# Performance work log

Hardware: AMD Instinct MI355X
Metric: run time of the kernel (lower is better)

The kernel has to match this reference:

```python
import jax, jax.numpy as jnp
import numpy as np

B, C, H, W_ = 64, 3, 224, 224
S = 196            # max_segments
MP = 400           # max_pixels_per_segment
D = 768            # embed_dim (vit_base)


def setup_inputs() -> dict:
    key = jax.random.key(0)
    k1, k2, k3 = jax.random.split(key, 3)
    img = jax.random.normal(k1, (B, C, H, W_), jnp.float32)
    segments = jax.random.randint(k2, (B, H, W_), 0, S, jnp.int32)
    W = jax.random.normal(k3, (C * MP, D), jnp.float32) * 0.02
    b = jnp.zeros((D,), jnp.float32)
    return {"img": img, "segments": segments, "W": W, "b": b}


def _embed_one(img_chw, seg_hw):
    """Gather up to MP pixels per segment (row-major order, like torch bool-mask
    indexing), zero-pad, and flatten in (C, MP) order. Returns [S, C*MP]."""
    c = img_chw.shape[0]
    P = H * W_
    seg = seg_hw.reshape(-1)                                   # [P]
    order = jnp.argsort(seg, stable=True)                      # pixels sorted by segment, row-major within segment
    sorted_seg = seg[order]
    counts = jax.ops.segment_sum(jnp.ones((P,), jnp.int32), seg, num_segments=S)
    starts = jnp.concatenate([jnp.zeros((1,), jnp.int32),
                              jnp.cumsum(counts)[:-1].astype(jnp.int32)])
    rank = jnp.arange(P, dtype=jnp.int32) - starts[sorted_seg]  # index within segment
    valid = rank < MP                                           # truncate overflow pixels
    safe_rank = jnp.minimum(rank, MP - 1)
    pix = img_chw.reshape(c, P).T[order]                        # [P, C]
    buf = jnp.zeros((S, MP, c), img_chw.dtype)
    # (segment, rank) pairs are unique for valid pixels; overflow adds zeros
    buf = buf.at[sorted_seg, safe_rank].add(pix * valid[:, None].astype(img_chw.dtype))
    # torch flattens (C, MP) row-major -> channel-major feature layout
    return buf.transpose(0, 2, 1).reshape(S, c * MP)


def reference(img, segments, W, b):
    feats = jax.vmap(_embed_one)(img, segments)  # [B, S, C*MP]
    return feats @ W + b                          # [B, S, D]
```

## Files before the change

kernel.cpp:

```cpp
#include <hip/hip_runtime.h>
#include <hip/hip_bf16.h>
#include <stdint.h>

#define BATCH 64
#define CHN 3
#define HH 224
#define WW 224
#define PIX (HH * WW)
#define NSEG 196
#define MAXP 400
#define KDIM (CHN * MAXP)
#define DN 768

#define KP4 1216
#define NTK 38
#define MROWS (BATCH * NSEG)

#define CHSZ 512
#define NCH (PIX / CHSZ)

typedef short short8 __attribute__((ext_vector_type(8)));
typedef float f32x4 __attribute__((ext_vector_type(4)));
typedef unsigned int uint4v __attribute__((ext_vector_type(4)));


__device__ __forceinline__ uint32_t packhl(float v) {
    uint32_t x = __float_as_uint(v);
    uint32_t hi = (x + 0x7FFFu + ((x >> 16) & 1u)) >> 16;
    float r = v - __uint_as_float(hi << 16);
    uint32_t y = __float_as_uint(r);
    uint32_t lo = (y + 0x7FFFu + ((y >> 16) & 1u)) >> 16;
    return (hi << 16) | lo;
}

__global__ void k_hist(const int* __restrict__ seg, int* __restrict__ hist) {
    __shared__ int cnt[NSEG];
    int blk = blockIdx.x;
    int b = blk / NCH, ch = blk % NCH;
    int tid = threadIdx.x;
    if (tid < NSEG) cnt[tid] = 0;
    __syncthreads();
    int s = seg[(size_t)b * PIX + ch * CHSZ + tid];
    atomicAdd(&cnt[s], 1);
    __syncthreads();
    if (tid < NSEG) hist[(size_t)blk * NSEG + tid] = cnt[tid];
}

__global__ void k_scan(int* __restrict__ hist, int* __restrict__ counts) {
    int i = blockIdx.x * blockDim.x + threadIdx.x;
    if (i >= BATCH * NSEG) return;
    int b = i / NSEG, s = i % NSEG;
    int run = 0;
    for (int c = 0; c < NCH; ++c) {
        size_t idx = ((size_t)b * NCH + c) * NSEG + s;
        int t = hist[idx];
        hist[idx] = run;
        run += t;
    }
    counts[i] = run;
}

__global__ void k_ztail(const int* __restrict__ counts, uint32_t* __restrict__ Apair) {
    int row = blockIdx.x * 4 + (threadIdx.x >> 6);
    int lane = threadIdx.x & 63;
    int cnt = counts[row];
    int start = 3 * min(cnt, MAXP);
    uint32_t* p = Apair + (size_t)row * KP4;
    for (int i = start + lane; i < KP4; i += 64) p[i] = 0u;
}

__global__ void k_scatter(const float* __restrict__ img,
                          const int* __restrict__ seg,
                          const int* __restrict__ offs,
                          uint32_t* __restrict__ Apair) {
    __shared__ int soff[NSEG];
    __shared__ int wcnt[8][NSEG];
    int blk = blockIdx.x;
    int b = blk / NCH, ch = blk % NCH;
    int tid = threadIdx.x;
    int lane = tid & 63, wid = tid >> 6;

    for (int i = tid; i < 8 * NSEG; i += CHSZ) ((int*)wcnt)[i] = 0;
    if (tid < NSEG) soff[tid] = offs[(size_t)blk * NSEG + tid];
    __syncthreads();

    int p = ch * CHSZ + tid;
    int sv = seg[(size_t)b * PIX + p];

    uint64_t m = ~0ull;
    #pragma unroll
    for (int bit = 0; bit < 8; ++bit) {
        uint64_t bal = __ballot((sv >> bit) & 1);
        m &= ((sv >> bit) & 1) ? bal : ~bal;
    }
    int before = __popcll(m & ((1ull << lane) - 1ull));
    int first  = __builtin_ctzll(m);
    if (lane == first) wcnt[wid][sv] = __popcll(m);
    __syncthreads();

    int base = soff[sv];
    for (int w2 = 0; w2 < wid; ++w2) base += wcnt[w2][sv];
    int r = base + before;

    if (r < MAXP) {
        const float* ib = img + (size_t)b * CHN * PIX + p;
        uint32_t* dst = Apair + (size_t)(b * NSEG + sv) * KP4 + 3 * r;
        uint32_t v0 = packhl(ib[0]);
        uint32_t v1 = packhl(ib[PIX]);
        uint32_t v2 = packhl(ib[2 * PIX]);
        dst[0] = v0; dst[1] = v1; dst[2] = v2;
    }
}

__global__ void k_wprep(const float* __restrict__ W, uint32_t* __restrict__ Wt) {
    __shared__ float t[32][33];
    int kt = blockIdx.x, nt = blockIdx.y;
    int tid = threadIdx.x;
    int tx = tid & 31, ty = tid >> 5;
    #pragma unroll
    for (int i = 0; i < 4; ++i) {
        int k = kt * 32 + i * 8 + ty;
        int n = nt * 32 + tx;
        t[i * 8 + ty][tx] = (k < KDIM) ? W[(size_t)k * DN + n] : 0.0f;
    }
    __syncthreads();
    #pragma unroll
    for (int i = 0; i < 4; ++i) {
        int n = nt * 32 + i * 8 + ty;
        int k = kt * 32 + tx;
        int kap = (k < KDIM) ? 3 * (k % MAXP) + (k / MAXP) : k;
        Wt[(size_t)n * KP4 + kap] = packhl(t[tx][i * 8 + ty]);
    }
}

__device__ __forceinline__ void gld16(const void* g, void* l) {
    __builtin_amdgcn_global_load_lds(
        (const __attribute__((address_space(1))) unsigned int*)g,
        (__attribute__((address_space(3))) unsigned int*)l, 16, 0, 0);
}

#define NWG 588
__global__ __launch_bounds__(256) void k_gemm(const uint32_t* __restrict__ A,
                                              const uint32_t* __restrict__ Bw,
                                              const float* __restrict__ bias,
                                              float* __restrict__ Co) {
    __shared__ uint32_t lds[2][2][128 * 32];
    int j = blockIdx.x;
    int xcd = j & 7, sl = j >> 3;
    const int q = NWG / 8, rm = NWG % 8;
    int wgid = (xcd < rm ? xcd * (q + 1) : rm * (q + 1) + (xcd - rm) * q) + sl;
    int bm = wgid / 6, bn = wgid % 6;

    int tid = threadIdx.x;
    int lane = tid & 63, w = tid >> 6;
    int wm = w >> 1, wn = w & 1;
    int srow = lane >> 3, sslot = lane & 7;
    int kb = lane >> 4, r15 = lane & 15;

    const uint32_t* Abase = A + (size_t)(bm * 128) * KP4;
    const uint32_t* Bbase = Bw + (size_t)(bn * 128) * KP4;

    f32x4 acc[4][4] = {};

#define STAGE(buf, kt) do {                                                   \
    _Pragma("unroll")                                                         \
    for (int qq = 0; qq < 4; ++qq) {                                          \
        int rb = (qq * 4 + w) * 8;                                            \
        int row = rb + srow;                                                  \
        int sp = sslot ^ (row & 7);                                           \
        gld16(Abase + (size_t)row * KP4 + (kt) * 32 + sp * 4,                 \
              &lds[buf][0][rb * 32]);                                         \
        gld16(Bbase + (size_t)row * KP4 + (kt) * 32 + sp * 4,                 \
              &lds[buf][1][rb * 32]);                                         \
    }                                                                         \
} while (0)

    STAGE(0, 0);
    __syncthreads();

    int cur = 0;
    for (int kt = 0; kt < NTK; ++kt) {
        if (kt + 1 < NTK) STAGE(cur ^ 1, kt + 1);

        short8 ah[4], al[4], bh[4], bl[4];
        #pragma unroll
        for (int mi = 0; mi < 4; ++mi) {
            int row = wm * 64 + mi * 16 + r15;
            int s0 = (2 * kb) ^ (row & 7), s1 = (2 * kb + 1) ^ (row & 7);
            uint4v w0 = *(const uint4v*)&lds[cur][0][row * 32 + s0 * 4];
            uint4v w1 = *(const uint4v*)&lds[cur][0][row * 32 + s1 * 4];
            union { uint32_t u[4]; short8 s; } H, L;
            H.u[0] = __builtin_amdgcn_perm(w0.y, w0.x, 0x07060302u);
            H.u[1] = __builtin_amdgcn_perm(w0.w, w0.z, 0x07060302u);
            H.u[2] = __builtin_amdgcn_perm(w1.y, w1.x, 0x07060302u);
            H.u[3] = __builtin_amdgcn_perm(w1.w, w1.z, 0x07060302u);
            L.u[0] = __builtin_amdgcn_perm(w0.y, w0.x, 0x05040100u);
            L.u[1] = __builtin_amdgcn_perm(w0.w, w0.z, 0x05040100u);
            L.u[2] = __builtin_amdgcn_perm(w1.y, w1.x, 0x05040100u);
            L.u[3] = __builtin_amdgcn_perm(w1.w, w1.z, 0x05040100u);
            ah[mi] = H.s; al[mi] = L.s;
        }
        #pragma unroll
        for (int ni = 0; ni < 4; ++ni) {
            int row = wn * 64 + ni * 16 + r15;
            int s0 = (2 * kb) ^ (row & 7), s1 = (2 * kb + 1) ^ (row & 7);
            uint4v w0 = *(const uint4v*)&lds[cur][1][row * 32 + s0 * 4];
            uint4v w1 = *(const uint4v*)&lds[cur][1][row * 32 + s1 * 4];
            union { uint32_t u[4]; short8 s; } H, L;
            H.u[0] = __builtin_amdgcn_perm(w0.y, w0.x, 0x07060302u);
            H.u[1] = __builtin_amdgcn_perm(w0.w, w0.z, 0x07060302u);
            H.u[2] = __builtin_amdgcn_perm(w1.y, w1.x, 0x07060302u);
            H.u[3] = __builtin_amdgcn_perm(w1.w, w1.z, 0x07060302u);
            L.u[0] = __builtin_amdgcn_perm(w0.y, w0.x, 0x05040100u);
            L.u[1] = __builtin_amdgcn_perm(w0.w, w0.z, 0x05040100u);
            L.u[2] = __builtin_amdgcn_perm(w1.y, w1.x, 0x05040100u);
            L.u[3] = __builtin_amdgcn_perm(w1.w, w1.z, 0x05040100u);
            bh[ni] = H.s; bl[ni] = L.s;
        }

        #pragma unroll
        for (int mi = 0; mi < 4; ++mi)
            #pragma unroll
            for (int ni = 0; ni < 4; ++ni) {
                acc[mi][ni] = __builtin_amdgcn_mfma_f32_16x16x32_bf16(
                    ah[mi], bh[ni], acc[mi][ni], 0, 0, 0);
                acc[mi][ni] = __builtin_amdgcn_mfma_f32_16x16x32_bf16(
                    al[mi], bh[ni], acc[mi][ni], 0, 0, 0);
                acc[mi][ni] = __builtin_amdgcn_mfma_f32_16x16x32_bf16(
                    ah[mi], bl[ni], acc[mi][ni], 0, 0, 0);
            }

        __syncthreads();
        cur ^= 1;
    }
#undef STAGE

    #pragma unroll
    for (int ni = 0; ni < 4; ++ni) {
        int col = bn * 128 + wn * 64 + ni * 16 + r15;
        float bv = bias[col];
        #pragma unroll
        for (int mi = 0; mi < 4; ++mi) {
            int rbase = bm * 128 + wm * 64 + mi * 16 + kb * 4;
            #pragma unroll
            for (int e = 0; e < 4; ++e)
                Co[(size_t)(rbase + e) * DN + col] = acc[mi][ni][e] + bv;
        }
    }
}

extern "C" void kernel_launch(void* const* d_in, const int* in_sizes, int n_in,
                              void* d_out, int out_size, void* d_ws, size_t ws_size,
                              hipStream_t stream) {
    const float* img = (const float*)d_in[0];
    const int*   seg = (const int*)d_in[1];
    const float* W   = (const float*)d_in[2];
    const float* bia = (const float*)d_in[3];
    float* out = (float*)d_out;

    const size_t APAIR_BYTES = (size_t)MROWS * KP4 * 4;
    const size_t HIST_BYTES  = (size_t)BATCH * NCH * NSEG * 4;
    uint32_t* Apair  = (uint32_t*)d_ws;
    int*      hist   = (int*)((char*)d_ws + APAIR_BYTES);
    int*      counts = (int*)((char*)d_ws + APAIR_BYTES + HIST_BYTES);
    uint32_t* Wt     = (uint32_t*)hist;

    k_hist<<<BATCH * NCH, CHSZ, 0, stream>>>(seg, hist);
    k_scan<<<(BATCH * NSEG + 255) / 256, 256, 0, stream>>>(hist, counts);
    k_ztail<<<MROWS / 4, 256, 0, stream>>>(counts, Apair);
    k_scatter<<<BATCH * NCH, CHSZ, 0, stream>>>(img, seg, hist, Apair);
    k_wprep<<<dim3(NTK, DN / 32), 256, 0, stream>>>(W, Wt);

    k_gemm<<<NWG, 256, 0, stream>>>(Apair, Wt, bia, out);
}
```

Before: 236.7 us.

## Restructure split-bf16 GEMM with half-swap MFMA pairing, parallel scan, XCD-remapped scatter

The GEMM now uses 512 threads (8 waves, 4x2 tiles each). It feeds the packed hi/lo bf16 words straight to MFMA, paired with a half-swapped B operand, so two MFMAs per tile give the full (ah+al)(bh+bl) product. This removes all the perm unpacking instructions but adds the al*bl term and changes the MFMA count and register pressure. The prefix scan changes from one thread per segment walking the chunks serially to one wavefront per segment using shuffle-based scans. The scatter kernel remaps block indices so neighbouring chunks land on the same XCD.

```diff
diff --git a/kernel.cpp b/kernel.cpp
--- a/kernel.cpp
+++ b/kernel.cpp
@@ -47,17 +47,23 @@
 }
 
 __global__ void k_scan(int* __restrict__ hist, int* __restrict__ counts) {
-    int i = blockIdx.x * blockDim.x + threadIdx.x;
-    if (i >= BATCH * NSEG) return;
-    int b = i / NSEG, s = i % NSEG;
-    int run = 0;
-    for (int c = 0; c < NCH; ++c) {
-        size_t idx = ((size_t)b * NCH + c) * NSEG + s;
-        int t = hist[idx];
-        hist[idx] = run;
-        run += t;
-    }
-    counts[i] = run;
+    int gw = blockIdx.x * 4 + (threadIdx.x >> 6);
+    int lane = threadIdx.x & 63;
+    int b = gw / NSEG, s = gw - b * NSEG;
+    size_t base = (size_t)b * NCH * NSEG + s;
+    int v0 = hist[base + (size_t)lane * NSEG];
+    int v1 = (lane < NCH - 64) ? hist[base + (size_t)(lane + 64) * NSEG] : 0;
+    int p0 = v0, p1 = v1;
+    #pragma unroll
+    for (int d = 1; d < 64; d <<= 1) {
+        int t0 = __shfl_up(p0, d);
+        int t1 = __shfl_up(p1, d);
+        if (lane >= d) { p0 += t0; p1 += t1; }
+    }
+    int tot0 = __shfl(p0, 63);
+    hist[base + (size_t)lane * NSEG] = p0 - v0;
+    if (lane < NCH - 64) hist[base + (size_t)(lane + 64) * NSEG] = tot0 + p1 - v1;
+    if (lane == NCH - 64 - 1) counts[gw] = tot0 + p1;
 }
 
 __global__ void k_ztail(const int* __restrict__ counts, uint32_t* __restrict__ Apair) {
@@ -75,13 +81,14 @@
                           uint32_t* __restrict__ Apair) {
     __shared__ int soff[NSEG];
     __shared__ int wcnt[8][NSEG];
-    int blk = blockIdx.x;
-    int b = blk / NCH, ch = blk % NCH;
+    int blk0 = blockIdx.x;
+    int wg = (blk0 & 7) * (BATCH * NCH / 8) + (blk0 >> 3);
+    int b = wg / NCH, ch = wg % NCH;
     int tid = threadIdx.x;
     int lane = tid & 63, wid = tid >> 6;
 
     for (int i = tid; i < 8 * NSEG; i += CHSZ) ((int*)wcnt)[i] = 0;
-    if (tid < NSEG) soff[tid] = offs[(size_t)blk * NSEG + tid];
+    if (tid < NSEG) soff[tid] = offs[(size_t)wg * NSEG + tid];
     __syncthreads();
 
     int p = ch * CHSZ + tid;
@@ -140,10 +147,10 @@
 }
 
 #define NWG 588
-__global__ __launch_bounds__(256) void k_gemm(const uint32_t* __restrict__ A,
-                                              const uint32_t* __restrict__ Bw,
-                                              const float* __restrict__ bias,
-                                              float* __restrict__ Co) {
+__global__ __launch_bounds__(512, 4) void k_gemm(const uint32_t* __restrict__ A,
+                                                 const uint32_t* __restrict__ Bw,
+                                                 const float* __restrict__ bias,
+                                                 float* __restrict__ Co) {
     __shared__ uint32_t lds[2][2][128 * 32];
     int j = blockIdx.x;
     int xcd = j & 7, sl = j >> 3;
@@ -153,26 +160,25 @@
 
     int tid = threadIdx.x;
     int lane = tid & 63, w = tid >> 6;
-    int wm = w >> 1, wn = w & 1;
-    int srow = lane >> 3, sslot = lane & 7;
-    int kb = lane >> 4, r15 = lane & 15;
-
-    const uint32_t* Abase = A + (size_t)(bm * 128) * KP4;
-    const uint32_t* Bbase = Bw + (size_t)(bn * 128) * KP4;
-
-    f32x4 acc[4][4] = {};
-
-#define STAGE(buf, kt) do {                                                   \
-    _Pragma("unroll")                                                         \
-    for (int qq = 0; qq < 4; ++qq) {                                          \
-        int rb = (qq * 4 + w) * 8;                                            \
-        int row = rb + srow;                                                  \
-        int sp = sslot ^ (row & 7);                                           \
-        gld16(Abase + (size_t)row * KP4 + (kt) * 32 + sp * 4,                 \
-              &lds[buf][0][rb * 32]);                                         \
-        gld16(Bbase + (size_t)row * KP4 + (kt) * 32 + sp * 4,                 \
-              &lds[buf][1][rb * 32]);                                         \
-    }                                                                         \
+    int wm = w >> 2, wn = w & 3;
+    int r15 = lane & 15, kb = lane >> 4;
+
+    int srow = w * 8 + (lane >> 3);
+    int sslot = lane & 7;
+    int ssw = sslot ^ (srow & 7);
+    size_t aoff0 = (size_t)srow * KP4 + ssw * 4;
+    size_t aoff1 = (size_t)(srow + 64) * KP4 + ssw * 4;
+
+    const uint32_t* Ab = A + (size_t)(bm * 128) * KP4;
+    const uint32_t* Bb = Bw + (size_t)(bn * 128) * KP4;
+
+    f32x4 acc[4][2] = {};
+
+#define STAGE(buf, kt) do {                                        \
+    gld16(Ab + aoff0 + (size_t)(kt) * 32, &lds[buf][0][w * 256]);  \
+    gld16(Ab + aoff1 + (size_t)(kt) * 32, &lds[buf][0][2048 + w * 256]); \
+    gld16(Bb + aoff0 + (size_t)(kt) * 32, &lds[buf][1][w * 256]);  \
+    gld16(Bb + aoff1 + (size_t)(kt) * 32, &lds[buf][1][2048 + w * 256]); \
 } while (0)
 
     STAGE(0, 0);
@@ -182,53 +188,34 @@
     for (int kt = 0; kt < NTK; ++kt) {
         if (kt + 1 < NTK) STAGE(cur ^ 1, kt + 1);
 
-        short8 ah[4], al[4], bh[4], bl[4];
         #pragma unroll
-        for (int mi = 0; mi < 4; ++mi) {
-            int row = wm * 64 + mi * 16 + r15;
-            int s0 = (2 * kb) ^ (row & 7), s1 = (2 * kb + 1) ^ (row & 7);
-            uint4v w0 = *(const uint4v*)&lds[cur][0][row * 32 + s0 * 4];
-            uint4v w1 = *(const uint4v*)&lds[cur][0][row * 32 + s1 * 4];
-            union { uint32_t u[4]; short8 s; } H, L;
-            H.u[0] = __builtin_amdgcn_perm(w0.y, w0.x, 0x07060302u);
-            H.u[1] = __builtin_amdgcn_perm(w0.w, w0.z, 0x07060302u);
-            H.u[2] = __builtin_amdgcn_perm(w1.y, w1.x, 0x07060302u);
-            H.u[3] = __builtin_amdgcn_perm(w1.w, w1.z, 0x07060302u);
-            L.u[0] = __builtin_amdgcn_perm(w0.y, w0.x, 0x05040100u);
-            L.u[1] = __builtin_amdgcn_perm(w0.w, w0.z, 0x05040100u);
-            L.u[2] = __builtin_amdgcn_perm(w1.y, w1.x, 0x05040100u);
-            L.u[3] = __builtin_amdgcn_perm(w1.w, w1.z, 0x05040100u);
-            ah[mi] = H.s; al[mi] = L.s;
+        for (int sg = 0; sg < 2; ++sg) {
+            union { uint4v u; short8 s; } af[4];
+            #pragma unroll
+            for (int mi = 0; mi < 4; ++mi) {
+                int row = wm * 64 + mi * 16 + r15;
+                int slot = (sg * 4 + kb) ^ (row & 7);
+                af[mi].u = *(const uint4v*)&lds[cur][0][row * 32 + slot * 4];
+            }
+            #pragma unroll
+            for (int ni = 0; ni < 2; ++ni) {
+                int row = wn * 32 + ni * 16 + r15;
+                int slot = (sg * 4 + kb) ^ (row & 7);
+                union { uint4v u; short8 s; } bf, bs;
+                bf.u = *(const uint4v*)&lds[cur][1][row * 32 + slot * 4];
+                bs.u.x = (bf.u.x >> 16) | (bf.u.x << 16);
+                bs.u.y = (bf.u.y >> 16) | (bf.u.y << 16);
+                bs.u.z = (bf.u.z >> 16) | (bf.u.z << 16);
+                bs.u.w = (bf.u.w >> 16) | (bf.u.w << 16);
+                #pragma unroll
+                for (int mi = 0; mi < 4; ++mi) {
+                    acc[mi][ni] = __builtin_amdgcn_mfma_f32_16x16x32_bf16(
+                        af[mi].s, bf.s, acc[mi][ni], 0, 0, 0);
+                    acc[mi][ni] = __builtin_amdgcn_mfma_f32_16x16x32_bf16(
+                        af[mi].s, bs.s, acc[mi][ni], 0, 0, 0);
+                }
+            }
         }
-        #pragma unroll
-        for (int ni = 0; ni < 4; ++ni) {
-            int row = wn * 64 + ni * 16 + r15;
-            int s0 = (2 * kb) ^ (row & 7), s1 = (2 * kb + 1) ^ (row & 7);
-            uint4v w0 = *(const uint4v*)&lds[cur][1][row * 32 + s0 * 4];
-            uint4v w1 = *(const uint4v*)&lds[cur][1][row * 32 + s1 * 4];
-            union { uint32_t u[4]; short8 s; } H, L;
-            H.u[0] = __builtin_amdgcn_perm(w0.y, w0.x, 0x07060302u);
-            H.u[1] = __builtin_amdgcn_perm(w0.w, w0.z, 0x07060302u);
-            H.u[2] = __builtin_amdgcn_perm(w1.y, w1.x, 0x07060302u);
-            H.u[3] = __builtin_amdgcn_perm(w1.w, w1.z, 0x07060302u);
-            L.u[0] = __builtin_amdgcn_perm(w0.y, w0.x, 0x05040100u);
-            L.u[1] = __builtin_amdgcn_perm(w0.w, w0.z, 0x05040100u);
-            L.u[2] = __builtin_amdgcn_perm(w1.y, w1.x, 0x05040100u);
-            L.u[3] = __builtin_amdgcn_perm(w1.w, w1.z, 0x05040100u);
-            bh[ni] = H.s; bl[ni] = L.s;
-        }
-
-        #pragma unroll
-        for (int mi = 0; mi < 4; ++mi)
-            #pragma unroll
-            for (int ni = 0; ni < 4; ++ni) {
-                acc[mi][ni] = __builtin_amdgcn_mfma_f32_16x16x32_bf16(
-                    ah[mi], bh[ni], acc[mi][ni], 0, 0, 0);
-                acc[mi][ni] = __builtin_amdgcn_mfma_f32_16x16x32_bf16(
-                    al[mi], bh[ni], acc[mi][ni], 0, 0, 0);
-                acc[mi][ni] = __builtin_amdgcn_mfma_f32_16x16x32_bf16(
-                    ah[mi], bl[ni], acc[mi][ni], 0, 0, 0);
-            }
 
         __syncthreads();
         cur ^= 1;
@@ -236,8 +223,8 @@
 #undef STAGE
 
     #pragma unroll
-    for (int ni = 0; ni < 4; ++ni) {
-        int col = bn * 128 + wn * 64 + ni * 16 + r15;
+    for (int ni = 0; ni < 2; ++ni) {
+        int col = bn * 128 + wn * 32 + ni * 16 + r15;
         float bv = bias[col];
         #pragma unroll
         for (int mi = 0; mi < 4; ++mi) {
@@ -266,10 +253,10 @@
     uint32_t* Wt     = (uint32_t*)hist;
 
     k_hist<<<BATCH * NCH, CHSZ, 0, stream>>>(seg, hist);
-    k_scan<<<(BATCH * NSEG + 255) / 256, 256, 0, stream>>>(hist, counts);
+    k_scan<<<MROWS / 4, 256, 0, stream>>>(hist, counts);
     k_ztail<<<MROWS / 4, 256, 0, stream>>>(counts, Apair);
     k_scatter<<<BATCH * NCH, CHSZ, 0, stream>>>(img, seg, hist, Apair);
     k_wprep<<<dim3(NTK, DN / 32), 256, 0, stream>>>(W, Wt);
 
-    k_gemm<<<NWG, 256, 0, stream>>>(Apair, Wt, bia, out);
-}
+    k_gemm<<<NWG, 512, 0, stream>>>(Apair, Wt, bia, out);
+}
```

After: 247.5 us. 4.6% more time.

## Switch GEMM to 32x32x16 MFMA with half-swapped B for split-bf16 products

Applied to the files above, without the earlier changes.

The split-bf16 GEMM now uses 32x32x16 MFMA tiles and feeds the packed hi|lo words straight in as the A operand. It pairs them with B once as-is and once with the halves swapped, so two MFMAs replace three and the perm unpacking is gone. The loop swaps __syncthreads for explicit vmcnt waits and raw s_barrier, and launch bounds request two workgroups per CU. The trade is that the two MFMAs also fold the hi/lo pairings into one dot product, which adds the lo*lo term harmlessly but relies on the packed layout lining up exactly.

```diff
diff --git a/kernel.cpp b/kernel.cpp
--- a/kernel.cpp
+++ b/kernel.cpp
@@ -20,7 +20,7 @@
 #define NCH (PIX / CHSZ)
 
 typedef short short8 __attribute__((ext_vector_type(8)));
-typedef float f32x4 __attribute__((ext_vector_type(4)));
+typedef float f32x16 __attribute__((ext_vector_type(16)));
 typedef unsigned int uint4v __attribute__((ext_vector_type(4)));
 
 
@@ -75,13 +75,13 @@
                           uint32_t* __restrict__ Apair) {
     __shared__ int soff[NSEG];
     __shared__ int wcnt[8][NSEG];
-    int blk = blockIdx.x;
-    int b = blk / NCH, ch = blk % NCH;
+    int wg = blockIdx.x;
+    int b = wg / NCH, ch = wg % NCH;
     int tid = threadIdx.x;
     int lane = tid & 63, wid = tid >> 6;
 
     for (int i = tid; i < 8 * NSEG; i += CHSZ) ((int*)wcnt)[i] = 0;
-    if (tid < NSEG) soff[tid] = offs[(size_t)blk * NSEG + tid];
+    if (tid < NSEG) soff[tid] = offs[(size_t)wg * NSEG + tid];
     __syncthreads();
 
     int p = ch * CHSZ + tid;
@@ -140,10 +140,10 @@
 }
 
 #define NWG 588
-__global__ __launch_bounds__(256) void k_gemm(const uint32_t* __restrict__ A,
-                                              const uint32_t* __restrict__ Bw,
-                                              const float* __restrict__ bias,
-                                              float* __restrict__ Co) {
+__global__ __launch_bounds__(256, 2) void k_gemm(const uint32_t* __restrict__ A,
+                                                 const uint32_t* __restrict__ Bw,
+                                                 const float* __restrict__ bias,
+                                                 float* __restrict__ Co) {
     __shared__ uint32_t lds[2][2][128 * 32];
     int j = blockIdx.x;
     int xcd = j & 7, sl = j >> 3;
@@ -154,97 +154,87 @@
     int tid = threadIdx.x;
     int lane = tid & 63, w = tid >> 6;
     int wm = w >> 1, wn = w & 1;
-    int srow = lane >> 3, sslot = lane & 7;
-    int kb = lane >> 4, r15 = lane & 15;
-
-    const uint32_t* Abase = A + (size_t)(bm * 128) * KP4;
-    const uint32_t* Bbase = Bw + (size_t)(bn * 128) * KP4;
-
-    f32x4 acc[4][4] = {};
+    int l31 = lane & 31, kh = lane >> 5;
+
+    const uint32_t* Ab = A + (size_t)(bm * 128) * KP4;
+    const uint32_t* Bb = Bw + (size_t)(bn * 128) * KP4;
+
+    f32x16 acc[2][2] = {};
+
+    int sr = lane >> 3, ss = lane & 7;
 
 #define STAGE(buf, kt) do {                                                   \
     _Pragma("unroll")                                                         \
     for (int qq = 0; qq < 4; ++qq) {                                          \
         int rb = (qq * 4 + w) * 8;                                            \
-        int row = rb + srow;                                                  \
-        int sp = sslot ^ (row & 7);                                           \
-        gld16(Abase + (size_t)row * KP4 + (kt) * 32 + sp * 4,                 \
+        int row = rb + sr;                                                    \
+        int sp = ss ^ (row & 7);                                              \
+        gld16(Ab + (size_t)row * KP4 + (size_t)(kt) * 32 + sp * 4,            \
               &lds[buf][0][rb * 32]);                                         \
-        gld16(Bbase + (size_t)row * KP4 + (kt) * 32 + sp * 4,                 \
+        gld16(Bb + (size_t)row * KP4 + (size_t)(kt) * 32 + sp * 4,            \
               &lds[buf][1][rb * 32]);                                         \
     }                                                                         \
 } while (0)
 
     STAGE(0, 0);
-    __syncthreads();
 
     int cur = 0;
     for (int kt = 0; kt < NTK; ++kt) {
-        if (kt + 1 < NTK) STAGE(cur ^ 1, kt + 1);
-
-        short8 ah[4], al[4], bh[4], bl[4];
+        if (kt + 1 < NTK) {
+            STAGE(cur ^ 1, kt + 1);
+            asm volatile("s_waitcnt vmcnt(8)" ::: "memory");
+        } else {
+            asm volatile("s_waitcnt vmcnt(0)" ::: "memory");
+        }
+        __builtin_amdgcn_s_barrier();
+
         #pragma unroll
-        for (int mi = 0; mi < 4; ++mi) {
-            int row = wm * 64 + mi * 16 + r15;
-            int s0 = (2 * kb) ^ (row & 7), s1 = (2 * kb + 1) ^ (row & 7);
-            uint4v w0 = *(const uint4v*)&lds[cur][0][row * 32 + s0 * 4];
-            uint4v w1 = *(const uint4v*)&lds[cur][0][row * 32 + s1 * 4];
-            union { uint32_t u[4]; short8 s; } H, L;
-            H.u[0] = __builtin_amdgcn_perm(w0.y, w0.x, 0x07060302u);
-            H.u[1] = __builtin_amdgcn_perm(w0.w, w0.z, 0x07060302u);
-            H.u[2] = __builtin_amdgcn_perm(w1.y, w1.x, 0x07060302u);
-            H.u[3] = __builtin_amdgcn_perm(w1.w, w1.z, 0x07060302u);
-            L.u[0] = __builtin_amdgcn_perm(w0.y, w0.x, 0x05040100u);
-            L.u[1] = __builtin_amdgcn_perm(w0.w, w0.z, 0x05040100u);
-            L.u[2] = __builtin_amdgcn_perm(w1.y, w1.x, 0x05040100u);
-            L.u[3] = __builtin_amdgcn_perm(w1.w, w1.z, 0x05040100u);
-            ah[mi] = H.s; al[mi] = L.s;
+        for (int ks = 0; ks < 4; ++ks) {
+            union { uint4v u; short8 s; } af[2], bf[2], bs[2];
+            #pragma unroll
+            for (int mi = 0; mi < 2; ++mi) {
+                int row = wm * 64 + mi * 32 + l31;
+                int slot = (ks * 2 + kh) ^ (row & 7);
+                af[mi].u = *(const uint4v*)&lds[cur][0][row * 32 + slot * 4];
+            }
+            #pragma unroll
+            for (int ni = 0; ni < 2; ++ni) {
+                int row = wn * 64 + ni * 32 + l31;
+                int slot = (ks * 2 + kh) ^ (row & 7);
+                bf[ni].u = *(const uint4v*)&lds[cur][1][row * 32 + slot * 4];
+                bs[ni].u.x = (bf[ni].u.x >> 16) | (bf[ni].u.x << 16);
+                bs[ni].u.y = (bf[ni].u.y >> 16) | (bf[ni].u.y << 16);
+                bs[ni].u.z = (bf[ni].u.z >> 16) | (bf[ni].u.z << 16);
+                bs[ni].u.w = (bf[ni].u.w >> 16) | (bf[ni].u.w << 16);
+            }
+            #pragma unroll
+            for (int mi = 0; mi < 2; ++mi)
+                #pragma unroll
+                for (int ni = 0; ni < 2; ++ni) {
+                    acc[mi][ni] = __builtin_amdgcn_mfma_f32_32x32x16_bf16(
+                        af[mi].s, bf[ni].s, acc[mi][ni], 0, 0, 0);
+                    acc[mi][ni] = __builtin_amdgcn_mfma_f32_32x32x16_bf16(
+                        af[mi].s, bs[ni].s, acc[mi][ni], 0, 0, 0);
+                }
         }
-        #pragma unroll
-        for (int ni = 0; ni < 4; ++ni) {
-            int row = wn * 64 + ni * 16 + r15;
-            int s0 = (2 * kb) ^ (row & 7), s1 = (2 * kb + 1) ^ (row & 7);
-            uint4v w0 = *(const uint4v*)&lds[cur][1][row * 32 + s0 * 4];
-            uint4v w1 = *(const uint4v*)&lds[cur][1][row * 32 + s1 * 4];
-            union { uint32_t u[4]; short8 s; } H, L;
-            H.u[0] = __builtin_amdgcn_perm(w0.y, w0.x, 0x07060302u);
-            H.u[1] = __builtin_amdgcn_perm(w0.w, w0.z, 0x07060302u);
-            H.u[2] = __builtin_amdgcn_perm(w1.y, w1.x, 0x07060302u);
-            H.u[3] = __builtin_amdgcn_perm(w1.w, w1.z, 0x07060302u);
-            L.u[0] = __builtin_amdgcn_perm(w0.y, w0.x, 0x05040100u);
-            L.u[1] = __builtin_amdgcn_perm(w0.w, w0.z, 0x05040100u);
-            L.u[2] = __builtin_amdgcn_perm(w1.y, w1.x, 0x05040100u);
-            L.u[3] = __builtin_amdgcn_perm(w1.w, w1.z, 0x05040100u);
-            bh[ni] = H.s; bl[ni] = L.s;
-        }
-
-        #pragma unroll
-        for (int mi = 0; mi < 4; ++mi)
-            #pragma unroll
-            for (int ni = 0; ni < 4; ++ni) {
-                acc[mi][ni] = __builtin_amdgcn_mfma_f32_16x16x32_bf16(
-                    ah[mi], bh[ni], acc[mi][ni], 0, 0, 0);
-                acc[mi][ni] = __builtin_amdgcn_mfma_f32_16x16x32_bf16(
-                    al[mi], bh[ni], acc[mi][ni], 0, 0, 0);
-                acc[mi][ni] = __builtin_amdgcn_mfma_f32_16x16x32_bf16(
-                    ah[mi], bl[ni], acc[mi][ni], 0, 0, 0);
-            }
-
-        __syncthreads();
+
+        __builtin_amdgcn_s_barrier();
         cur ^= 1;
     }
 #undef STAGE
 
     #pragma unroll
-    for (int ni = 0; ni < 4; ++ni) {
-        int col = bn * 128 + wn * 64 + ni * 16 + r15;
+    for (int ni = 0; ni < 2; ++ni) {
+        int col = bn * 128 + wn * 64 + ni * 32 + l31;
         float bv = bias[col];
         #pragma unroll
-        for (int mi = 0; mi < 4; ++mi) {
-            int rbase = bm * 128 + wm * 64 + mi * 16 + kb * 4;
-            #pragma unroll
-            for (int e = 0; e < 4; ++e)
-                Co[(size_t)(rbase + e) * DN + col] = acc[mi][ni][e] + bv;
+        for (int mi = 0; mi < 2; ++mi) {
+            int rb = bm * 128 + wm * 64 + mi * 32 + 4 * kh;
+            #pragma unroll
+            for (int reg = 0; reg < 16; ++reg) {
+                int row = rb + (reg & 3) + 8 * (reg >> 2);
+                Co[(size_t)row * DN + col] = acc[mi][ni][reg] + bv;
+            }
         }
     }
 }
```

Result: slower. 255.6 us (+8.0%).
